# Performance work log

Hardware: AMD Instinct MI355X
Metric: run time of the kernel (lower is better)

The kernel has to match this reference:

```python
import math
import jax, jax.numpy as jnp
import numpy as np

INP_MODES = [4, 8, 8, 4]   # prod = 1024 = in_features
OUT_MODES = [8, 8, 8, 8]   # prod = 4096 = out_features
TT_RANKS = [1, 8, 8, 8, 1]
IN_FEATURES = 1024
OUT_FEATURES = 4096
BATCH = 8192
D = len(INP_MODES)


def setup_inputs() -> dict:
    key = jax.random.key(0)
    ks = jax.random.split(key, D + 2)
    inp = {"x": jax.random.normal(ks[0], (BATCH, IN_FEATURES), dtype=jnp.float32)}
    for i in range(D):
        # xavier_normal per the module's reset_parameters
        fan_in = TT_RANKS[i] * INP_MODES[i]
        fan_out = TT_RANKS[i + 1] * OUT_MODES[i]
        std = math.sqrt(2.0 / (fan_in + fan_out))
        shape = (TT_RANKS[i] * OUT_MODES[i], TT_RANKS[i + 1] * INP_MODES[i])
        inp[f"core{i}"] = std * jax.random.normal(ks[i + 1], shape, dtype=jnp.float32)
    bound = 1.0 / math.sqrt(IN_FEATURES)
    inp["bias"] = jax.random.uniform(ks[D + 1], (OUT_FEATURES,), dtype=jnp.float32,
                                     minval=-bound, maxval=bound)
    return inp


def _tt_forward(x, cores, bias):
    # x: [B, in_features]. Sequentially contract input modes against TT cores.
    # Invariant after step i: h has shape (B, M=prod(m_0..m_i), r_{i+1}, N=prod(n_{i+1}..))
    B = x.shape[0]
    h = x.reshape(B, 1, 1, IN_FEATURES)
    for i, c in enumerate(cores):
        r, m, q, n = TT_RANKS[i], OUT_MODES[i], TT_RANKS[i + 1], INP_MODES[i]
        c4 = c.reshape(r, m, q, n)          # (r_i, m_i, r_{i+1}, n_i)
        M = h.shape[1]
        h = h.reshape(B, M, r, n, -1)       # split current input mode n_i
        # contract rank r_i and input mode n_i; produce out mode m_i (s) and next rank q
        h = jnp.einsum('bmrnp,rsqn->bmsqp', h, c4)
        h = h.reshape(B, M * m, q, -1)
    y = h.reshape(B, OUT_FEATURES) + bias
    return y


def reference(x, core0, core1, core2, core3, bias):
    return _tt_forward(x, [core0, core1, core2, core3], bias)
```

## Files before the change

kernel.cpp:

```cpp
#include <hip/hip_runtime.h>
#include <hip/hip_bf16.h>

typedef __bf16 bf16x4 __attribute__((ext_vector_type(4)));
typedef __bf16 bf16x8 __attribute__((ext_vector_type(8)));
typedef float  f32x4  __attribute__((ext_vector_type(4)));
typedef float  f32x16 __attribute__((ext_vector_type(16)));

#define MFMA32(a,b,c) __builtin_amdgcn_mfma_f32_32x32x16_bf16((a),(b),(c),0,0,0)


__global__ __launch_bounds__(256) void tt_kernel(
    const float* __restrict__ x,  const float* __restrict__ c0,
    const float* __restrict__ c1, const float* __restrict__ c2,
    const float* __restrict__ c3, const float* __restrict__ bias,
    float* __restrict__ y)
{
    __shared__ __align__(16) __bf16 w23l[16384];
    __shared__ __align__(16) __bf16 xt[2048];
    __shared__ __align__(16) __bf16 hb[16384];

    const int tid  = threadIdx.x;
    const int wid  = tid >> 6;
    const int lane = tid & 63;
    const int hh   = lane >> 5;
    const int c32  = lane & 31;
    const int rt   = wid & 1;
    const int ct   = wid >> 1;

    {
      const int r = tid >> 2, kb = (tid & 3) * 64;
      const int m2 = r >> 3, m3 = r & 7;
      float c3v[8][4];
      #pragma unroll
      for (int r3 = 0; r3 < 8; ++r3)
        #pragma unroll
        for (int n3 = 0; n3 < 4; ++n3)
          c3v[r3][n3] = c3[(r3 * 8 + m3) * 4 + n3];
      for (int j = 0; j < 64; ++j) {
        const int k = kb + j;
        const int n2 = k >> 5, n3 = (k >> 3) & 3, r2 = k & 7;
        float s = 0.f;
        #pragma unroll
        for (int r3 = 0; r3 < 8; ++r3)
          s += c2[(r2 * 8 + m2) * 64 + r3 * 8 + n2] * c3v[r3][n3];
        w23l[r * 256 + (((k >> 3) ^ (r & 31)) << 3) + (k & 7)] = (__bf16)s;
      }
    }

    bf16x8 w01f[8][2];
    {
      const int row = rt * 32 + c32, m1 = row >> 3, r2w = row & 7;
      float c1row[8][8];
      #pragma unroll
      for (int r1 = 0; r1 < 8; ++r1)
        #pragma unroll
        for (int n1 = 0; n1 < 8; ++n1)
          c1row[r1][n1] = c1[(r1 * 8 + m1) * 64 + r2w * 8 + n1];
      for (int m0 = 0; m0 < 8; ++m0) {
        #pragma unroll
        for (int kt = 0; kt < 2; ++kt) {
          const int n0 = kt * 2 + hh;
          #pragma unroll
          for (int j = 0; j < 8; ++j) {
            float s = 0.f;
            #pragma unroll
            for (int r1 = 0; r1 < 8; ++r1)
              s += c0[m0 * 32 + r1 * 4 + n0] * c1row[r1][j];
            w01f[m0][kt][j] = (__bf16)s;
          }
        }
      }
    }

    for (int it = 0; it < 8; ++it) {
      const int b0 = (blockIdx.x * 8 + it) * 2;

      {
        const int bsel = tid >> 7, col = tid & 31, k0q = (tid >> 5) & 3;
        const float* xp = x + (size_t)(b0 + bsel) * 1024 + col;
        bf16x8 v;
        #pragma unroll
        for (int j = 0; j < 8; ++j) v[j] = (__bf16)xp[(k0q * 8 + j) * 32];
        *(bf16x8*)&xt[(bsel * 32 + col) * 32 + ((k0q ^ (col & 3)) << 3)] = v;
      }
      __syncthreads();

      bf16x8 xf[2];
      #pragma unroll
      for (int kt = 0; kt < 2; ++kt)
        xf[kt] = *(const bf16x8*)
          &xt[(ct * 32 + c32) * 32 + (((kt * 2 + hh) ^ (c32 & 3)) << 3)];

      #pragma unroll
      for (int q = 0; q < 2; ++q) {
        #pragma unroll
        for (int m0h = 0; m0h < 4; ++m0h) {
          f32x16 acc = {};
          acc = MFMA32(w01f[q * 4 + m0h][0], xf[0], acc);
          acc = MFMA32(w01f[q * 4 + m0h][1], xf[1], acc);
          #pragma unroll
          for (int p = 0; p < 4; ++p) {
            bf16x4 o;
            #pragma unroll
            for (int i = 0; i < 4; ++i) o[i] = (__bf16)acc[p * 4 + i];
            const int cl = ct * 32 + m0h * 8 + rt * 4 + p;
            *(bf16x4*)&hb[cl * 256 + ((c32 ^ (cl & 31)) << 3) + hh * 4] = o;
          }
        }
        __syncthreads();

        const __bf16* arow = &w23l[(rt * 32 + c32) * 256];
        const __bf16* brow = &hb[(ct * 32 + c32) * 256];
        f32x16 acc2 = {};
        #pragma unroll
        for (int kt = 0; kt < 16; ++kt) {
          const int op = ((kt * 2 + hh) ^ c32) << 3;
          const bf16x8 af = *(const bf16x8*)&arow[op];
          const bf16x8 bf = *(const bf16x8*)&brow[op];
          acc2 = MFMA32(af, bf, acc2);
        }

        const size_t ybase = (size_t)(b0 + ct) * 4096;
        const int boff = (q * 4 + (c32 >> 3)) * 512 + (c32 & 7) * 64 + hh * 4;
        #pragma unroll
        for (int p = 0; p < 4; ++p) {
          const int off = boff + (rt * 4 + p) * 8;
          const f32x4 bv = *(const f32x4*)&bias[off];
          f32x4 o;
          #pragma unroll
          for (int i = 0; i < 4; ++i) o[i] = acc2[p * 4 + i] + bv[i];
          *(f32x4*)&y[ybase + off] = o;
        }
        __syncthreads();
      }
    }
}

extern "C" void kernel_launch(void* const* d_in, const int* in_sizes, int n_in,
                              void* d_out, int out_size, void* d_ws, size_t ws_size,
                              hipStream_t stream) {
    const float* x    = (const float*)d_in[0];
    const float* c0   = (const float*)d_in[1];
    const float* c1   = (const float*)d_in[2];
    const float* c2   = (const float*)d_in[3];
    const float* c3   = (const float*)d_in[4];
    const float* bias = (const float*)d_in[5];
    float* yout = (float*)d_out;
    tt_kernel<<<512, 256, 0, stream>>>(x, c0, c1, c2, c3, bias, yout);
}
```

Baseline: 227.9 us.

## Prefetch next x tile into registers, split MFMA accumulators, transpose output stores

Loads the next iteration's x rows into registers during the current iteration's first MFMA stage and writes them to LDS late, so one barrier per iteration goes away and global load latency is hidden. Replaces __syncthreads with an explicit LDS-only waitcnt plus s_barrier, so barriers no longer wait on outstanding global stores. Splits the second GEMM into two independent accumulators to shorten the MFMA dependency chain. Swaps the MFMA operand order so each lane stores scalar floats coalesced across lanes, and preloads bias into registers. The cost is higher register pressure and narrower scalar stores in place of 16-byte vector stores.

```diff
diff --git a/kernel.cpp b/kernel.cpp
--- a/kernel.cpp
+++ b/kernel.cpp
@@ -7,6 +7,8 @@
 typedef float  f32x16 __attribute__((ext_vector_type(16)));
 
 #define MFMA32(a,b,c) __builtin_amdgcn_mfma_f32_32x32x16_bf16((a),(b),(c),0,0,0)
+
+#define BAR_LDS() asm volatile("s_waitcnt lgkmcnt(0)\n\ts_barrier" ::: "memory")
 
 
 __global__ __launch_bounds__(256) void tt_kernel(
@@ -72,18 +74,32 @@
       }
     }
 
+    float bv[2][4][4];
+    #pragma unroll
+    for (int q = 0; q < 2; ++q)
+      #pragma unroll
+      for (int p = 0; p < 4; ++p)
+        #pragma unroll
+        for (int i = 0; i < 4; ++i)
+          bv[q][p][i] = bias[q * 2048 + p * 512 + (hh * 4 + i) * 64 + rt * 32 + c32];
+
+    const int bsel = tid >> 7, xcol = tid & 31, k0q = (tid >> 5) & 3;
+    const int xtoff = (bsel * 32 + xcol) * 32 + ((k0q ^ (xcol & 3)) << 3);
+
+    float xv[8];
+    {
+      const float* xp = x + (size_t)(blockIdx.x * 16 + bsel) * 1024 + xcol;
+      #pragma unroll
+      for (int j = 0; j < 8; ++j) xv[j] = xp[(k0q * 8 + j) * 32];
+      bf16x8 v;
+      #pragma unroll
+      for (int j = 0; j < 8; ++j) v[j] = (__bf16)xv[j];
+      *(bf16x8*)&xt[xtoff] = v;
+    }
+    BAR_LDS();
+
     for (int it = 0; it < 8; ++it) {
       const int b0 = (blockIdx.x * 8 + it) * 2;
-
-      {
-        const int bsel = tid >> 7, col = tid & 31, k0q = (tid >> 5) & 3;
-        const float* xp = x + (size_t)(b0 + bsel) * 1024 + col;
-        bf16x8 v;
-        #pragma unroll
-        for (int j = 0; j < 8; ++j) v[j] = (__bf16)xp[(k0q * 8 + j) * 32];
-        *(bf16x8*)&xt[(bsel * 32 + col) * 32 + ((k0q ^ (col & 3)) << 3)] = v;
-      }
-      __syncthreads();
 
       bf16x8 xf[2];
       #pragma unroll
@@ -93,6 +109,13 @@
 
       #pragma unroll
       for (int q = 0; q < 2; ++q) {
+        if (q == 0) {
+          const int itn = (it + 1) & 7;
+          const float* xp = x + (size_t)((blockIdx.x * 8 + itn) * 2 + bsel) * 1024 + xcol;
+          #pragma unroll
+          for (int j = 0; j < 8; ++j) xv[j] = xp[(k0q * 8 + j) * 32];
+        }
+
         #pragma unroll
         for (int m0h = 0; m0h < 4; ++m0h) {
           f32x16 acc = {};
@@ -107,31 +130,36 @@
             *(bf16x4*)&hb[cl * 256 + ((c32 ^ (cl & 31)) << 3) + hh * 4] = o;
           }
         }
-        __syncthreads();
+        BAR_LDS();
 
         const __bf16* arow = &w23l[(rt * 32 + c32) * 256];
         const __bf16* brow = &hb[(ct * 32 + c32) * 256];
-        f32x16 acc2 = {};
+        f32x16 acc2a = {}, acc2b = {};
         #pragma unroll
-        for (int kt = 0; kt < 16; ++kt) {
-          const int op = ((kt * 2 + hh) ^ c32) << 3;
-          const bf16x8 af = *(const bf16x8*)&arow[op];
-          const bf16x8 bf = *(const bf16x8*)&brow[op];
-          acc2 = MFMA32(af, bf, acc2);
+        for (int kt = 0; kt < 16; kt += 2) {
+          const int op0 = ((kt * 2 + hh) ^ c32) << 3;
+          const int op1 = ((kt * 2 + 2 + hh) ^ c32) << 3;
+          acc2a = MFMA32(*(const bf16x8*)&brow[op0], *(const bf16x8*)&arow[op0], acc2a);
+          acc2b = MFMA32(*(const bf16x8*)&brow[op1], *(const bf16x8*)&arow[op1], acc2b);
         }
 
-        const size_t ybase = (size_t)(b0 + ct) * 4096;
-        const int boff = (q * 4 + (c32 >> 3)) * 512 + (c32 & 7) * 64 + hh * 4;
-        #pragma unroll
-        for (int p = 0; p < 4; ++p) {
-          const int off = boff + (rt * 4 + p) * 8;
-          const f32x4 bv = *(const f32x4*)&bias[off];
-          f32x4 o;
+        if (q == 1) {
+          bf16x8 v;
           #pragma unroll
-          for (int i = 0; i < 4; ++i) o[i] = acc2[p * 4 + i] + bv[i];
-          *(f32x4*)&y[ybase + off] = o;
+          for (int j = 0; j < 8; ++j) v[j] = (__bf16)xv[j];
+          *(bf16x8*)&xt[xtoff] = v;
         }
-        __syncthreads();
+
+        {
+          const size_t ybase = (size_t)(b0 + ct) * 4096 + q * 2048 + rt * 32 + c32;
+          #pragma unroll
+          for (int p = 0; p < 4; ++p)
+            #pragma unroll
+            for (int i = 0; i < 4; ++i)
+              y[ybase + p * 512 + (hh * 4 + i) * 64] =
+                  (acc2a[p * 4 + i] + acc2b[p * 4 + i]) + bv[q][p][i];
+        }
+        BAR_LDS();
       }
     }
 }
```

Measured after the change: 210.8 us. 1.08x faster.
